# Kernel tuning notes

Hardware: AMD Instinct MI355X
Metric: run time of the kernel (lower is better)

The kernel has to match this reference:

```python
import jax, jax.numpy as jnp
import numpy as np

B, T, HID = 2, 1024, 768
EXPAND, NH, HD, NG, NS, K = 2, 24, 64, 1, 128, 4
INTER = EXPAND * HID            # 1536
CONV_DIM = INTER + 2 * NG * NS  # 1792
NLVL = 15                       # get_num_levels(16384, base=2)
EPS = 1e-5


def _levels(T):
    # Fenwick-style hierarchical level matrix (HType.WEAK, base 2):
    # level(t, s) = 0 on the diagonal, else msb(t XOR s) + 1.
    t = np.arange(T)
    x = t[:, None] ^ t[None, :]
    lev = np.zeros((T, T), np.int32)
    nz = x > 0
    lev[nz] = np.floor(np.log2(x[nz])).astype(np.int32) + 1
    return lev

_LEV = jnp.asarray(_levels(T))  # [T,T] int32, values in [0, NLVL)


def setup_inputs() -> dict:
    key = jax.random.key(0)
    ks = jax.random.split(key, 4)
    P = INTER + CONV_DIM + NH * (NLVL + 1)  # 3712
    return {
        "hidden_states": jax.random.normal(ks[0], (B, T, HID), jnp.float32),
        "in_proj_w": jax.random.normal(ks[1], (P, HID), jnp.float32) * (HID ** -0.5),
        "conv_w": jax.random.normal(ks[2], (CONV_DIM, 1, K), jnp.float32) * 0.2,
        "conv_b": jnp.zeros((CONV_DIM,), jnp.float32),
        "dt_bias": jnp.ones((NH,), jnp.float32),
        "A_log": jnp.log(jnp.arange(1, NH + 1, dtype=jnp.float32)),
        "L": jnp.ones((NH, NLVL), jnp.float32),
        "D": jnp.ones((NH,), jnp.float32),
        "norm_weight": jnp.ones((INTER,), jnp.float32),
        "out_proj_w": jax.random.normal(ks[3], (HID, INTER), jnp.float32) * (INTER ** -0.5),
    }


def reference(hidden_states, in_proj_w, conv_w, conv_b, dt_bias, A_log, L, D,
              norm_weight, out_proj_w):
    # in_proj and split: [gate | xBC | dt | dl]
    proj = hidden_states @ in_proj_w.T                       # [B,T,P]
    gate = proj[..., :INTER]
    xBC = proj[..., INTER:INTER + CONV_DIM]
    dt = proj[..., INTER + CONV_DIM:INTER + CONV_DIM + NH]
    dl = proj[..., INTER + CONV_DIM + NH:].reshape(B, T, NH, NLVL)

    # fused causal depthwise conv1d + SiLU
    xBC = jax.lax.conv_general_dilated(
        xBC.transpose(0, 2, 1), conv_w, window_strides=(1,),
        padding=[(K - 1, 0)], dimension_numbers=("NCH", "OIH", "NCH"),
        feature_group_count=CONV_DIM) + conv_b[None, :, None]
    xBC = jax.nn.silu(xBC.transpose(0, 2, 1))                # [B,T,CONV_DIM]

    x = xBC[..., :INTER].reshape(B, T, NH, HD)               # [B,T,H,P]
    Bm = xBC[..., INTER:INTER + NG * NS].reshape(B, T, NG, NS)
    Cm = xBC[..., INTER + NG * NS:].reshape(B, T, NG, NS)
    hpg = NH // NG
    Bh = jnp.repeat(Bm, hpg, axis=2)                         # [B,T,H,N]
    Ch = jnp.repeat(Cm, hpg, axis=2)

    dt = jax.nn.softplus(dt + dt_bias)                       # [B,T,H]
    A = -jnp.exp(A_log)                                      # [H]
    cumA = jnp.cumsum(dt * A, axis=1)                        # [B,T,H]

    # semiseparable decay exp(sum_{s<r<=t} dt_r * A), causal-masked
    cA = cumA.transpose(0, 2, 1)                             # [B,H,T]
    diff = cA[:, :, :, None] - cA[:, :, None, :]             # [B,H,T,T]
    mask = jnp.tril(jnp.ones((T, T), bool))
    decay = jnp.exp(jnp.where(mask[None, None], diff, -1e9))

    CB = jnp.einsum("bthn,bshn->bhts", Ch, Bh)               # [B,H,T,T]

    # hierarchical lambda gating: positive lambda, per-head learned scale L
    lam = jax.nn.softplus(dl) * L                            # [B,T,H,NLVL]
    lam_g = jnp.take_along_axis(lam.transpose(0, 2, 1, 3),
                                _LEV[None, None], axis=-1)   # [B,H,T,T]

    M = CB * decay * lam_g * dt.transpose(0, 2, 1)[:, :, None, :]
    y = jnp.einsum("bhts,bshp->bthp", M, x)                  # [B,T,H,P]
    y = y + D[None, None, :, None] * x
    y = y.reshape(B, T, INTER)

    # gated RMSNorm (norm_before_gate=False): norm(y * silu(gate))
    y = y * jax.nn.silu(gate)
    var = jnp.mean(jnp.square(y), axis=-1, keepdims=True)
    y = y * jax.lax.rsqrt(var + EPS) * norm_weight

    return y @ out_proj_w.T                                  # [B,T,HID]
```

## Files before the change

kernel.cpp:

```cpp
#include <hip/hip_runtime.h>
#include <hip/hip_bf16.h>
#include <math.h>

#define B_ 2
#define T_ 1024
#define HID_ 768
#define INTER_ 1536
#define NH_ 24
#define HD_ 64
#define NS_ 128
#define NLVL_ 15
#define CONV_DIM_ 1792
#define P_ 3712
#define EPS_ 1e-5f

typedef short short8_t __attribute__((ext_vector_type(8)));
typedef short short4_t __attribute__((ext_vector_type(4)));
typedef float float4_t __attribute__((ext_vector_type(4)));


__device__ __forceinline__ float softplus_f(float x) {
  return (x > 20.f) ? x : log1pf(__expf(x));
}
__device__ __forceinline__ short f2bf(float f) {
  union { float f; unsigned u; } v; v.f = f;
  unsigned r = v.u + 0x7FFF + ((v.u >> 16) & 1);
  return (short)(r >> 16);
}
__device__ __forceinline__ float bf2f(short s) {
  union { unsigned u; float f; } v; v.u = ((unsigned)(unsigned short)s) << 16;
  return v.f;
}
__device__ __forceinline__ void gl_lds16(const void* g, void* l) {
  __builtin_amdgcn_global_load_lds(
      (const __attribute__((address_space(1))) unsigned int*)g,
      (__attribute__((address_space(3))) unsigned int*)l, 16, 0, 0);
}

__global__ __launch_bounds__(256) void cvtdt_k(
    const float* __restrict__ hs, const float* __restrict__ Win, const float* __restrict__ Wout,
    short* __restrict__ hsbf, short* __restrict__ wibf, short* __restrict__ wobf,
    float* __restrict__ dtraw, int ncvt)
{
  const long na = (long)B_ * T_ * HID_, nb = (long)P_ * HID_, nc = (long)HID_ * INTER_;
  if ((int)blockIdx.x < ncvt) {
    const long i = ((long)blockIdx.x * 256 + threadIdx.x) * 8;
    const float* src; short* dst; long off;
    if (i < na)           { src = hs;   dst = hsbf; off = i; }
    else if (i < na + nb) { src = Win;  dst = wibf; off = i - na; }
    else if (i < na + nb + nc) { src = Wout; dst = wobf; off = i - na - nb; }
    else return;
    const long base = (off & ~31L) + ((off >> 3) & 3) * 4;
    float4 v0 = *(const float4*)(src + base);
    float4 v1 = *(const float4*)(src + base + 16);
    short8_t o;
    o[0] = f2bf(v0.x); o[1] = f2bf(v0.y); o[2] = f2bf(v0.z); o[3] = f2bf(v0.w);
    o[4] = f2bf(v1.x); o[5] = f2bf(v1.y); o[6] = f2bf(v1.z); o[7] = f2bf(v1.w);
    *(short8_t*)(dst + off) = o;
  } else {
    const int rowbt = ((int)blockIdx.x - ncvt) * 4 + (threadIdx.x >> 6);
    const int lane = threadIdx.x & 63;
    float hv[12];
    const float* hrow = hs + (long)rowbt * HID_ + lane * 12;
    #pragma unroll
    for (int j = 0; j < 12; j++) hv[j] = hrow[j];
    const float* wbase = Win + (long)(INTER_ + CONV_DIM_) * HID_ + lane * 12;
    for (int h = 0; h < NH_; h++) {
      const float* wr = wbase + (long)h * HID_;
      float s = 0.f;
      #pragma unroll
      for (int j = 0; j < 12; j++) s = fmaf(hv[j], wr[j], s);
      #pragma unroll
      for (int off = 32; off; off >>= 1) s += __shfl_xor(s, off);
      if (lane == 0) dtraw[(long)rowbt * NH_ + h] = s;
    }
  }
}

__device__ __forceinline__ short8_t ldfrag(const short* Ts, int row, int lg) {
  return *(const short8_t*)(Ts + row * 32 + lg * 8);
}

__device__ __forceinline__ short8_t ldfrag64(const short* Ts, int row, int kk, int lg) {
  const int cc = (kk * 4 + lg) ^ (row & 7);
  return *(const short8_t*)(Ts + row * 64 + cc * 8);
}

__global__ __launch_bounds__(256) void inproj_scan_k(
    const short* __restrict__ A, const short* __restrict__ B, short* __restrict__ C,
    const float* __restrict__ dtraw, const float* __restrict__ dt_bias,
    const float* __restrict__ A_log, float* __restrict__ dtT, float* __restrict__ cAT,
    float* __restrict__ qT)
{
  constexpr int TM = 128, TN = 128, K = HID_, BK = 64;
  constexpr int PSZ = TM * 32;
  constexpr int ASZ = 2 * PSZ;
  __shared__ short As[2 * ASZ];
  __shared__ short Bs[2 * ASZ];

  if (blockIdx.y >= 16) {
    const int sid = ((int)blockIdx.y - 16) * 29 + (int)blockIdx.x;
    if (sid >= B_ * NH_) return;
    const int b = sid / NH_;
    const int h = sid % NH_;
    const float bias = dt_bias[h];
    const float Ah = -__expf(A_log[h]);
    const long ob = (long)(h * B_ + b) * T_;
    float* sc = (float*)As;
    float carry = 0.f;
    for (int c0 = 0; c0 < T_; c0 += 256) {
      const int t = c0 + threadIdx.x;
      const long bt = (long)b * T_ + t;
      float sp = softplus_f(dtraw[bt * NH_ + h] + bias);
      dtT[ob + t] = sp;
      sc[threadIdx.x] = sp * Ah;
      __syncthreads();
      for (int off = 1; off < 256; off <<= 1) {
        float add = (threadIdx.x >= off) ? sc[threadIdx.x - off] : 0.f;
        __syncthreads();
        sc[threadIdx.x] += add;
        __syncthreads();
      }
      cAT[ob + t] = carry + sc[threadIdx.x];
      qT[ob + t] = sp * __expf(sc[threadIdx.x | 63] - sc[threadIdx.x]);
      float tot = sc[255];
      __syncthreads();
      carry += tot;
    }
    return;
  }

  const int tid = threadIdx.x;
  const int w = tid >> 6, lane = tid & 63;
  const int lr = lane & 15, lg = lane >> 4;
  const int wr = w >> 1, wc = w & 1;
  const int m0 = blockIdx.y * TM, n0 = blockIdx.x * TN;
  const int srow = lane >> 2;
  const int sc2 = (lane & 3) * 8;

  auto stage = [&](int buf, int k0) {
    #pragma unroll
    for (int it = 0; it < 2; it++) {
      const int cb = w + 4 * it;
      const int row = cb * 16 + srow;
      #pragma unroll
      for (int kg = 0; kg < 2; kg++) {
        gl_lds16(A + (long)(m0 + row) * K + k0 + kg * 32 + sc2,
                 As + buf * ASZ + kg * PSZ + cb * 512);
        gl_lds16(B + (long)(n0 + row) * K + k0 + kg * 32 + sc2,
                 Bs + buf * ASZ + kg * PSZ + cb * 512);
      }
    }
  };

  float4_t acc[4][4] = {};
  int cur = 0;
  stage(0, 0);
  for (int k0 = 0; k0 < K; k0 += BK) {
    __syncthreads();
    if (k0 + BK < K) stage(cur ^ 1, k0 + BK);
    #pragma unroll
    for (int kg = 0; kg < 2; kg++) {
      const short* Ab = As + cur * ASZ + kg * PSZ;
      const short* Bb = Bs + cur * ASZ + kg * PSZ;
      short8_t af[4], bf[4];
      #pragma unroll
      for (int m = 0; m < 4; m++) af[m] = ldfrag(Ab, wr * 64 + m * 16 + lr, lg);
      #pragma unroll
      for (int n = 0; n < 4; n++) bf[n] = ldfrag(Bb, wc * 64 + n * 16 + lr, lg);
      #pragma unroll
      for (int m = 0; m < 4; m++)
        #pragma unroll
        for (int n = 0; n < 4; n++)
          acc[m][n] = __builtin_amdgcn_mfma_f32_16x16x32_bf16(af[m], bf[n], acc[m][n], 0, 0, 0);
    }
    cur ^= 1;
  }

  #pragma unroll
  for (int m = 0; m < 4; m++)
    #pragma unroll
    for (int n = 0; n < 4; n++)
      #pragma unroll
      for (int r = 0; r < 4; r++) {
        const int row = m0 + wr * 64 + m * 16 + lg * 4 + r;
        const int col = n0 + wc * 64 + n * 16 + lr;
        C[(long)row * P_ + col] = f2bf(acc[m][n][r]);
      }
}

__global__ __launch_bounds__(256) void gemm_out_k(
    const short* __restrict__ A, const short* __restrict__ B, float* __restrict__ C,
    int M, int N, int K)
{
  constexpr int PSZ = 64 * 32;
  constexpr int BKG = 4;
  constexpr int BUF = PSZ * BKG;
  __shared__ short As[2 * BUF];
  __shared__ short Bs[2 * BUF];
  const int tid = threadIdx.x;
  const int w = tid >> 6, lane = tid & 63;
  const int lr = lane & 15, lg = lane >> 4;
  const int wr = w >> 1, wc = w & 1;
  const int m0 = blockIdx.y * 64, n0 = blockIdx.x * 64;
  const int srow = lane >> 2;
  const int sc = (lane & 3) * 8;

  auto stage = [&](int buf, int k0) {
    const int row = w * 16 + srow;
    #pragma unroll
    for (int kg = 0; kg < BKG; kg++) {
      gl_lds16(A + (long)(m0 + row) * K + k0 + kg * 32 + sc, As + buf * BUF + kg * PSZ + w * 512);
      gl_lds16(B + (long)(n0 + row) * K + k0 + kg * 32 + sc, Bs + buf * BUF + kg * PSZ + w * 512);
    }
  };

  float4_t acc[2][2] = {};
  int cur = 0;
  stage(0, 0);
  for (int k0 = 0; k0 < K; k0 += 128) {
    __syncthreads();
    if (k0 + 128 < K) stage(cur ^ 1, k0 + 128);
    #pragma unroll
    for (int kg = 0; kg < BKG; kg++) {
      const short* Ab = As + cur * BUF + kg * PSZ;
      const short* Bb = Bs + cur * BUF + kg * PSZ;
      short8_t af[2], bf[2];
      #pragma unroll
      for (int m = 0; m < 2; m++) af[m] = ldfrag(Ab, wr * 32 + m * 16 + lr, lg);
      #pragma unroll
      for (int n = 0; n < 2; n++) bf[n] = ldfrag(Bb, wc * 32 + n * 16 + lr, lg);
      #pragma unroll
      for (int m = 0; m < 2; m++)
        #pragma unroll
        for (int n = 0; n < 2; n++)
          acc[m][n] = __builtin_amdgcn_mfma_f32_16x16x32_bf16(af[m], bf[n], acc[m][n], 0, 0, 0);
    }
    cur ^= 1;
  }

  #pragma unroll
  for (int m = 0; m < 2; m++)
    #pragma unroll
    for (int n = 0; n < 2; n++)
      #pragma unroll
      for (int r = 0; r < 4; r++) {
        const int row = m0 + wr * 32 + m * 16 + lg * 4 + r;
        const int col = n0 + wc * 32 + n * 16 + lr;
        C[(long)row * N + col] = acc[m][n][r];
      }
}

__global__ __launch_bounds__(256) void gemm_cbh_k(
    const short* __restrict__ Chh, const short* __restrict__ Bh, short* __restrict__ CBh)
{
  if (blockIdx.x > blockIdx.y) return;
  Chh += (long)blockIdx.z * T_ * NS_;
  Bh  += (long)blockIdx.z * T_ * NS_;
  CBh += (long)blockIdx.z * T_ * T_;
  constexpr int PSZ = 64 * 32;
  __shared__ short As[4 * PSZ];
  __shared__ short Bs[4 * PSZ];
  const int tid = threadIdx.x;
  const int w = tid >> 6, lane = tid & 63;
  const int lr = lane & 15, lg = lane >> 4;
  const int wr = w >> 1, wc = w & 1;
  const int m0 = blockIdx.y * 64, n0 = blockIdx.x * 64;
  const int srow = lane >> 2;
  const int sc = (lane & 3) * 8;

  {
    const int row = w * 16 + srow;
    #pragma unroll
    for (int kg = 0; kg < 4; kg++) {
      gl_lds16(Chh + (long)(m0 + row) * NS_ + kg * 32 + sc, As + kg * PSZ + w * 512);
      gl_lds16(Bh  + (long)(n0 + row) * NS_ + kg * 32 + sc, Bs + kg * PSZ + w * 512);
    }
  }
  __syncthreads();

  float4_t acc[2][2] = {};
  #pragma unroll
  for (int kg = 0; kg < 4; kg++) {
    const short* Ab = As + kg * PSZ;
    const short* Bb = Bs + kg * PSZ;
    short8_t af[2], bf[2];
    #pragma unroll
    for (int m = 0; m < 2; m++) af[m] = ldfrag(Ab, wr * 32 + m * 16 + lr, lg);
    #pragma unroll
    for (int n = 0; n < 2; n++) bf[n] = ldfrag(Bb, wc * 32 + n * 16 + lr, lg);
    #pragma unroll
    for (int m = 0; m < 2; m++)
      #pragma unroll
      for (int n = 0; n < 2; n++)
        acc[m][n] = __builtin_amdgcn_mfma_f32_16x16x32_bf16(af[m], bf[n], acc[m][n], 0, 0, 0);
  }

  #pragma unroll
  for (int m = 0; m < 2; m++)
    #pragma unroll
    for (int n = 0; n < 2; n++)
      #pragma unroll
      for (int r = 0; r < 4; r++) {
        const int row = m0 + wr * 32 + m * 16 + lg * 4 + r;
        const int sl = wc * 32 + n * 16 + lr;
        const int g = sl >> 5, k32 = sl & 31;
        const int cc = g * 4 + ((k32 >> 2) & 3);
        const int off = ((cc ^ (row & 7)) * 8) + 4 * (k32 >> 4) + (k32 & 3);
        CBh[(long)row * T_ + n0 + off] = f2bf(acc[m][n][r]);
      }
}

__global__ __launch_bounds__(256) void conv_silu_k(
    const short* __restrict__ projh, const float* __restrict__ cw, const float* __restrict__ cbias,
    const float* __restrict__ qT,
    short* __restrict__ xTr, short* __restrict__ xTq,
    short* __restrict__ Bh, short* __restrict__ Chh)
{
  const int c0 = blockIdx.x * 256;
  const int t0 = blockIdx.y * 16;
  const int b  = blockIdx.z;
  const int tid = threadIdx.x;
  __shared__ float S[19][256];
  #pragma unroll
  for (int r = 0; r < 19; r++) {
    const int t = t0 - 3 + r;
    S[r][tid] = (t >= 0) ? bf2f(projh[((long)b * T_ + t) * P_ + INTER_ + c0 + tid]) : 0.f;
  }
  __syncthreads();
  const int c = c0 + tid;
  const float4 w = *(const float4*)(cw + c * 4);
  const float bias = cbias[c];
  float acc[16];
  #pragma unroll
  for (int tt = 0; tt < 16; tt++) {
    float a = bias + w.w * S[tt + 3][tid] + w.z * S[tt + 2][tid]
                   + w.y * S[tt + 1][tid] + w.x * S[tt][tid];
    acc[tt] = a / (1.f + __expf(-a));
  }
  if (c < INTER_) {
    const int h = c >> 6, hd = c & 63;
    const long chb = (long)(h * B_ + b) * T_;
    float qv[16];
    #pragma unroll
    for (int qq = 0; qq < 4; qq++) {
      float4 q4 = *(const float4*)(qT + chb + t0 + qq * 4);
      qv[qq*4+0] = q4.x; qv[qq*4+1] = q4.y; qv[qq*4+2] = q4.z; qv[qq*4+3] = q4.w;
    }
    const long base = ((long)(b * NH_ + h) * HD_ + hd) * T_ + (t0 & ~63);
    const int g = (t0 >> 5) & 1, h2 = (t0 >> 4) & 1, sw = hd & 7;
    #pragma unroll
    for (int a = 0; a < 4; a++) {
      short4_t xr, xq;
      #pragma unroll
      for (int r = 0; r < 4; r++) {
        xr[r] = f2bf(acc[a * 4 + r]);
        xq[r] = f2bf(acc[a * 4 + r] * qv[a * 4 + r]);
      }
      const int off = (((g * 4 + a) ^ sw) * 8) + h2 * 4;
      *(short4_t*)(xTr + base + off) = xr;
      *(short4_t*)(xTq + base + off) = xq;
    }
  } else {
    const int ch0 = c - INTER_;
    const bool isB = ch0 < NS_;
    const int k = isB ? ch0 : ch0 - NS_;
    const int k32 = k & 31;
    const int P = (k & ~31) + 8 * ((k32 >> 2) & 3) + 4 * (k32 >> 4) + (k32 & 3);
    short* dst = isB ? Bh : Chh;
    #pragma unroll
    for (int tt = 0; tt < 16; tt++) {
      const long bt = (long)b * T_ + t0 + tt;
      dst[bt * NS_ + P] = f2bf(acc[tt]);
    }
  }
}

__global__ __launch_bounds__(256) void attn_mfma3_k(
    const short* __restrict__ xTr, const short* __restrict__ xTq,
    const short* __restrict__ CBh,
    const float* __restrict__ cAT, const float* __restrict__ dtT,
    const short* __restrict__ projh, const float* __restrict__ Lw,
    const float* __restrict__ Dv,
    short* __restrict__ ybh)
{
  const int h = blockIdx.x;
  const int tt = (T_ / 64 - 1) - blockIdx.y;
  const int b = blockIdx.z;
  const int t0 = tt * 64;
  const int tid = threadIdx.x;
  const int w = tid >> 6, lane = tid & 63;
  const int lr = lane & 15, lg = lane >> 4;

  __shared__ short CBl[2][64 * 64];
  __shared__ short Xl[2][64 * 64];
  __shared__ float lamS[64][17];

  for (int f = tid; f < 64 * NLVL_; f += 256) {
    int r = f / NLVL_, l = f - r * NLVL_;
    lamS[r][l] = softplus_f(
        bf2f(projh[((long)b * T_ + t0 + r) * P_ + INTER_ + CONV_DIM_ + NH_ + h * NLVL_ + l]))
        * Lw[h * NLVL_ + l];
  }

  const int tl = w * 16 + lr;
  const int t  = t0 + tl;
  const int orow = w * 16 + lg * 4;
  const long chb = (long)(h * B_ + b) * T_;
  const float catv = cAT[chb + t];
  float cao[4];
  #pragma unroll
  for (int r = 0; r < 4; r++) cao[r] = cAT[chb + t0 + orow + r];

  const short* xbr = xTr + (long)(b * NH_ + h) * HD_ * T_;
  const short* xbq = xTq + (long)(b * NH_ + h) * HD_ * T_;
  const short* CBbase = CBh + (long)b * T_ * T_ + (long)t0 * T_;

  const int srow = w * 16 + (lane >> 3);
  const int sch = (lane & 7) * 8;

  auto stage = [&](int buf, int st) {
    const int s0 = st * 64;
    const short* xsrc = (st == tt) ? xbr : xbq;
    #pragma unroll
    for (int i = 0; i < 2; i++) {
      gl_lds16(CBbase + (long)(srow + i * 8) * T_ + s0 + sch, &CBl[buf][(w * 16 + i * 8) * 64]);
      gl_lds16(xsrc + (long)(srow + i * 8) * T_ + s0 + sch, &Xl[buf][(w * 16 + i * 8) * 64]);
    }
  };

  float4_t acc[4] = {};
  int cur = 0;
  stage(0, 0);
  for (int st = 0; st <= tt; st++) {
    __syncthreads();
    if (st < tt) stage(cur ^ 1, st + 1);
    const int s0 = st * 64;
    if (st < tt) {
      const float caE = cAT[chb + s0 + 63];
      const int lev = 32 - __clz(t0 ^ s0);
      float k1o[4];
      #pragma unroll
      for (int r = 0; r < 4; r++)
        k1o[r] = __expf(cao[r] - caE) * lamS[orow + r][lev];
      float4_t dtile[4] = {};
      __builtin_amdgcn_s_setprio(1);
      #pragma unroll
      for (int kk = 0; kk < 2; kk++) {
        short8_t af = ldfrag64(CBl[cur], tl, kk, lg);
        #pragma unroll
        for (int n = 0; n < 4; n++) {
          short8_t bfv = ldfrag64(Xl[cur], n * 16 + lr, kk, lg);
          dtile[n] = __builtin_amdgcn_mfma_f32_16x16x32_bf16(af, bfv, dtile[n], 0, 0, 0);
        }
      }
      __builtin_amdgcn_s_setprio(0);
      #pragma unroll
      for (int n = 0; n < 4; n++)
        #pragma unroll
        for (int r = 0; r < 4; r++)
          acc[n][r] = fmaf(k1o[r], dtile[n][r], acc[n][r]);
    } else {
      #pragma unroll
      for (int kk = 0; kk < 2; kk++) {
        short8_t cb8 = ldfrag64(CBl[cur], tl, kk, lg);
        short8_t af;
        #pragma unroll
        for (int g = 0; g < 2; g++) {
          const int sb = s0 + kk * 32 + g * 16 + lg * 4;
          float4_t ca4 = *(const float4_t*)(cAT + chb + sb);
          float4_t dt4 = *(const float4_t*)(dtT + chb + sb);
          #pragma unroll
          for (int a = 0; a < 4; a++) {
            const int sg = sb + a;
            float m = 0.f;
            if (sg <= t) {
              const int xo = t ^ sg;
              const int lev2 = xo ? (32 - __clz(xo)) : 0;
              m = bf2f(cb8[g * 4 + a]) * __expf(catv - ca4[a]) * lamS[tl][lev2] * dt4[a];
            }
            af[g * 4 + a] = f2bf(m);
          }
        }
        __builtin_amdgcn_s_setprio(1);
        #pragma unroll
        for (int n = 0; n < 4; n++) {
          short8_t bfv = ldfrag64(Xl[cur], n * 16 + lr, kk, lg);
          acc[n] = __builtin_amdgcn_mfma_f32_16x16x32_bf16(af, bfv, acc[n], 0, 0, 0);
        }
        __builtin_amdgcn_s_setprio(0);
      }
    }
    cur ^= 1;
  }

  const float Dh = Dv[h];
  const short* Xd = Xl[cur ^ 1];
  #pragma unroll
  for (int n = 0; n < 4; n++) {
    #pragma unroll
    for (int r = 0; r < 4; r++) {
      const int trow = t0 + orow + r;
      const int hd = n * 16 + lr;
      const int xoff = hd * 64 + ((((w >> 1) * 4 + lg) ^ (hd & 7)) * 8) + (w & 1) * 4 + r;
      const float xv = bf2f(Xd[xoff]);
      ybh[((long)b * T_ + trow) * INTER_ + h * HD_ + hd] = f2bf(acc[n][r] + Dh * xv);
    }
  }
}

__global__ __launch_bounds__(192) void gate_rms_k(
    const short* __restrict__ ybh, const short* __restrict__ projh,
    const float* __restrict__ nw, short* __restrict__ ynorm)
{
  const long bt = blockIdx.x;
  const short* gp = projh + bt * P_;
  const short* yp = ybh + bt * INTER_;
  const int i = threadIdx.x;
  const int lo = (i >> 2) * 32 + (i & 3) * 4;
  const int hi = lo + 16;
  float v[8];
  float ss = 0.f;
  {
    short4_t g0 = *(const short4_t*)(gp + lo);
    short4_t g1 = *(const short4_t*)(gp + hi);
    short4_t y0 = *(const short4_t*)(yp + lo);
    short4_t y1 = *(const short4_t*)(yp + hi);
    float ga[8] = {bf2f(g0[0]), bf2f(g0[1]), bf2f(g0[2]), bf2f(g0[3]),
                   bf2f(g1[0]), bf2f(g1[1]), bf2f(g1[2]), bf2f(g1[3])};
    float ya[8] = {bf2f(y0[0]), bf2f(y0[1]), bf2f(y0[2]), bf2f(y0[3]),
                   bf2f(y1[0]), bf2f(y1[1]), bf2f(y1[2]), bf2f(y1[3])};
    #pragma unroll
    for (int j = 0; j < 8; j++) {
      float val = ya[j] * (ga[j] / (1.f + __expf(-ga[j])));
      v[j] = val;
      ss += val * val;
    }
  }
  #pragma unroll
  for (int off = 32; off > 0; off >>= 1) ss += __shfl_xor(ss, off);
  __shared__ float part[3];
  if ((i & 63) == 0) part[i >> 6] = ss;
  __syncthreads();
  const float tot = part[0] + part[1] + part[2];
  const float r = rsqrtf(tot * (1.f / INTER_) + EPS_);
  short8_t o;
  #pragma unroll
  for (int j = 0; j < 8; j++) {
    const int idx = (j < 4) ? (lo + j) : (hi + j - 4);
    o[j] = f2bf(v[j] * r * nw[idx]);
  }
  *(short8_t*)(ynorm + bt * INTER_ + i * 8) = o;
}

extern "C" void kernel_launch(void* const* d_in, const int* in_sizes, int n_in,
                              void* d_out, int out_size, void* d_ws, size_t ws_size,
                              hipStream_t stream) {
  const float* hs   = (const float*)d_in[0];
  const float* Win  = (const float*)d_in[1];
  const float* cw   = (const float*)d_in[2];
  const float* cb   = (const float*)d_in[3];
  const float* dtb  = (const float*)d_in[4];
  const float* Alog = (const float*)d_in[5];
  const float* Lw   = (const float*)d_in[6];
  const float* Dv   = (const float*)d_in[7];
  const float* nw   = (const float*)d_in[8];
  const float* Wout = (const float*)d_in[9];
  float* out = (float*)d_out;

  const long n_hs = (long)B_ * T_ * HID_;
  const long n_wi = (long)P_ * HID_;
  const long n_wo = (long)HID_ * INTER_;

  float* ws = (float*)d_ws;
  long o = 0;
  float* projreg = ws + o; o += (long)B_ * T_ * P_ / 2 + 16;
  short* xbf   = (short*)(ws + o); o += (long)B_ * T_ * INTER_ / 2;
  short* Bh    = (short*)(ws + o); o += (long)B_ * T_ * NS_ / 2;
  short* Chh   = (short*)(ws + o); o += (long)B_ * T_ * NS_ / 2;
  float* dtT   = ws + o; o += (long)B_ * T_ * NH_;
  float* cAT   = ws + o; o += (long)B_ * T_ * NH_;
  float* qT    = ws + o; o += (long)B_ * T_ * NH_;
  float* dtraw = ws + o; o += (long)B_ * T_ * NH_;
  short* CBh   = (short*)(ws + o); o += (long)B_ * T_ * T_ / 2;
  short* ybh   = (short*)(ws + o); o += (long)B_ * T_ * INTER_ / 2;
  float* yxreg = ws + o; o += (long)B_ * T_ * INTER_ / 2;
  short* hsbf  = (short*)(ws + o); o += n_hs / 2;
  short* wibf  = (short*)(ws + o); o += n_wi / 2;
  short* wobf  = (short*)(ws + o); o += n_wo / 2;
  short* projh = (short*)projreg;
  short* xTr   = (short*)yxreg;
  short* ynrmb = (short*)yxreg;
  short* xTq   = hsbf;
  (void)xbf;

  const int ncvt = (int)((n_hs + n_wi + n_wo) / 8 / 256);

  cvtdt_k<<<ncvt + (B_ * T_) / 4, 256, 0, stream>>>(
      hs, Win, Wout, hsbf, wibf, wobf, dtraw, ncvt);
  inproj_scan_k<<<dim3(P_ / 128, 18), 256, 0, stream>>>(
      hsbf, wibf, projh, dtraw, dtb, Alog, dtT, cAT, qT);
  conv_silu_k<<<dim3(CONV_DIM_ / 256, T_ / 16, B_), 256, 0, stream>>>(
      projh, cw, cb, qT, xTr, xTq, Bh, Chh);
  gemm_cbh_k<<<dim3(T_ / 64, T_ / 64, B_), 256, 0, stream>>>(Chh, Bh, CBh);
  attn_mfma3_k<<<dim3(NH_, T_ / 64, B_), 256, 0, stream>>>(
      xTr, xTq, CBh, cAT, dtT, projh, Lw, Dv, ybh);
  gate_rms_k<<<B_ * T_, 192, 0, stream>>>(ybh, projh, nw, ynrmb);
  gemm_out_k<<<dim3(HID_ / 64, (B_ * T_) / 64), 256, 0, stream>>>(
      ynrmb, wobf, out, B_ * T_, HID_, INTER_);
}
```

Before: 110.1 us.

## Triple-buffer attention tile staging with explicit vmcnt waits; vectorize conv loads

The attention kernel moves from double to triple buffering of the CB and X tiles. It prefetches two stages ahead and uses explicit s_waitcnt vmcnt plus a raw s_barrier instead of __syncthreads, so global-to-LDS loads overlap more with MFMA work. Per-tile cA end values are preloaded into shared memory rather than read from global memory inside the loop. The conv kernel's input staging now uses 16-byte vector loads of eight bf16 values per thread instead of scalar loads. The costs are more LDS use, which may reduce occupancy, and fragile hand-written wait counts that depend on how many loads each stage issues.

```diff
diff --git a/kernel.cpp b/kernel.cpp
--- a/kernel.cpp
+++ b/kernel.cpp
@@ -322,10 +322,17 @@
   const int b  = blockIdx.z;
   const int tid = threadIdx.x;
   __shared__ float S[19][256];
-  #pragma unroll
-  for (int r = 0; r < 19; r++) {
+  for (int q = tid; q < 19 * 32; q += 256) {
+    const int r = q >> 5, c8 = (q & 31) * 8;
     const int t = t0 - 3 + r;
-    S[r][tid] = (t >= 0) ? bf2f(projh[((long)b * T_ + t) * P_ + INTER_ + c0 + tid]) : 0.f;
+    float4 f0 = {0.f, 0.f, 0.f, 0.f}, f1 = {0.f, 0.f, 0.f, 0.f};
+    if (t >= 0) {
+      short8_t v = *(const short8_t*)(projh + ((long)b * T_ + t) * P_ + INTER_ + c0 + c8);
+      f0.x = bf2f(v[0]); f0.y = bf2f(v[1]); f0.z = bf2f(v[2]); f0.w = bf2f(v[3]);
+      f1.x = bf2f(v[4]); f1.y = bf2f(v[5]); f1.z = bf2f(v[6]); f1.w = bf2f(v[7]);
+    }
+    *(float4*)(&S[r][c8])     = f0;
+    *(float4*)(&S[r][c8 + 4]) = f1;
   }
   __syncthreads();
   const int c = c0 + tid;
@@ -392,21 +399,23 @@
   const int w = tid >> 6, lane = tid & 63;
   const int lr = lane & 15, lg = lane >> 4;
 
-  __shared__ short CBl[2][64 * 64];
-  __shared__ short Xl[2][64 * 64];
+  __shared__ short CBl[3][64 * 64];
+  __shared__ short Xl[3][64 * 64];
   __shared__ float lamS[64][17];
-
+  __shared__ float caEs[16];
+
+  const long chb = (long)(h * B_ + b) * T_;
   for (int f = tid; f < 64 * NLVL_; f += 256) {
     int r = f / NLVL_, l = f - r * NLVL_;
     lamS[r][l] = softplus_f(
         bf2f(projh[((long)b * T_ + t0 + r) * P_ + INTER_ + CONV_DIM_ + NH_ + h * NLVL_ + l]))
         * Lw[h * NLVL_ + l];
   }
+  if (tid < 16) caEs[tid] = cAT[chb + tid * 64 + 63];
 
   const int tl = w * 16 + lr;
   const int t  = t0 + tl;
   const int orow = w * 16 + lg * 4;
-  const long chb = (long)(h * B_ + b) * T_;
   const float catv = cAT[chb + t];
   float cao[4];
   #pragma unroll
@@ -430,14 +439,20 @@
   };
 
   float4_t acc[4] = {};
-  int cur = 0;
   stage(0, 0);
+  if (tt >= 1) stage(1, 1);
+  asm volatile("s_waitcnt lgkmcnt(0)" ::: "memory");
+
   for (int st = 0; st <= tt; st++) {
-    __syncthreads();
-    if (st < tt) stage(cur ^ 1, st + 1);
+    if (st < tt) asm volatile("s_waitcnt vmcnt(4)" ::: "memory");
+    else         asm volatile("s_waitcnt vmcnt(0)" ::: "memory");
+    __builtin_amdgcn_s_barrier();
+    __builtin_amdgcn_sched_barrier(0);
+    if (st + 2 <= tt) stage((st + 2) % 3, st + 2);
+    const int cur = st % 3;
     const int s0 = st * 64;
     if (st < tt) {
-      const float caE = cAT[chb + s0 + 63];
+      const float caE = caEs[st];
       const int lev = 32 - __clz(t0 ^ s0);
       float k1o[4];
       #pragma unroll
@@ -491,11 +506,10 @@
         __builtin_amdgcn_s_setprio(0);
       }
     }
-    cur ^= 1;
   }
 
   const float Dh = Dv[h];
-  const short* Xd = Xl[cur ^ 1];
+  const short* Xd = Xl[tt % 3];
   #pragma unroll
   for (int n = 0; n < 4; n++) {
     #pragma unroll
```

Result: faster. 107.4 us (median of 3 runs) (-2.5%).
